# Kernel optimization log

Measured on AMD Instinct MI355X. Metric: run time of the kernel, lower is better.

## Reference

```python
import jax, jax.numpy as jnp
import numpy as np

B, T, D = 2, 1024, 2048
E, K, H = 64, 4, 512          # n_experts, top-k, expert_dim
S, HS = 2, H * K              # shared experts, shared hidden dim
CAP = 512


def setup_inputs() -> dict:
    key = jax.random.key(0)
    ks = jax.random.split(key, 9)
    scale = 0.02
    return {
        "x": jax.random.normal(ks[0], (B, T, D), jnp.float32),
        "Wr": jax.random.normal(ks[1], (D, E), jnp.float32) * scale,
        "router_bias": jnp.zeros((E,), jnp.float32),
        "Wg": jax.random.normal(ks[2], (E, D, H), jnp.float32) * scale,
        "Wu": jax.random.normal(ks[3], (E, D, H), jnp.float32) * scale,
        "Wd": jax.random.normal(ks[4], (E, H, D), jnp.float32) * scale,
        "Sg": jax.random.normal(ks[5], (S, D, HS), jnp.float32) * scale,
        "Su": jax.random.normal(ks[6], (S, D, HS), jnp.float32) * scale,
        "Sd": jax.random.normal(ks[7], (S, HS, D), jnp.float32) * scale,
    }


def reference(x, Wr, router_bias, Wg, Wu, Wd, Sg, Su, Sd):
    Bx, Tx, Dx = x.shape
    N = Bx * Tx
    flat = x.reshape(N, Dx)                              # [N, D]

    # ---- router ----
    logits = flat @ Wr + router_bias                     # [N, E]
    scores = jax.nn.softmax(logits, axis=-1)
    topk_scores, topk_idx = jax.lax.top_k(scores, K)     # [N, K]
    topk_scores = topk_scores / topk_scores.sum(-1, keepdims=True)

    eid = topk_idx.reshape(-1)                           # [N*K] expert per assignment
    w = topk_scores.reshape(-1)                          # [N*K] combine weight
    tok = jnp.repeat(jnp.arange(N), K)                   # [N*K] source token id

    # position of each assignment within its expert's buffer
    oh = jax.nn.one_hot(eid, E, dtype=jnp.int32)         # [N*K, E]
    pos = ((jnp.cumsum(oh, axis=0) * oh).sum(-1) - 1)    # [N*K]
    valid = pos < CAP

    # ---- dispatch: scatter tokens into per-expert buffers ----
    xb = jnp.zeros((E, CAP, Dx), x.dtype).at[eid, pos].set(flat[tok], mode="drop")

    # ---- grouped SwiGLU expert FFN ----
    h = jax.nn.silu(jnp.einsum("ecd,edh->ech", xb, Wg)) * jnp.einsum("ecd,edh->ech", xb, Wu)
    yb = jnp.einsum("ech,ehd->ecd", h, Wd)               # [E, CAP, D]

    # ---- combine: gather back and weighted scatter-add to tokens ----
    y = yb[eid, jnp.minimum(pos, CAP - 1)] * (w * valid)[:, None]
    out = jnp.zeros((N, Dx), x.dtype).at[tok].add(y)

    # ---- always-on shared experts ----
    hs = jax.nn.silu(jnp.einsum("nd,sdh->nsh", flat, Sg)) * jnp.einsum("nd,sdh->nsh", flat, Su)
    out = out + jnp.einsum("nsh,shd->nd", hs, Sd)

    return out.reshape(Bx, Tx, Dx)
```

## Files before the change

### kernel.cpp

```cpp
#include <hip/hip_runtime.h>
#include <hip/hip_bf16.h>
#include <stdint.h>

#define N_TOK 2048
#define DM    2048
#define NEXP  64
#define TOPK  4
#define HEXP  512
#define CAPC  512
#define NSH   2
#define HSH   2048
#define RTB   8

typedef __attribute__((ext_vector_type(8))) short short8;
typedef __attribute__((ext_vector_type(4))) float f32x4;
typedef __attribute__((ext_vector_type(4))) float f4;
typedef __attribute__((ext_vector_type(4))) unsigned uint4v;

#define GLDS16(g, l) __builtin_amdgcn_global_load_lds(                     \
    (const __attribute__((address_space(1))) void*)(g),                    \
    (__attribute__((address_space(3))) void*)(l), 16, 0, 0)

#define VMWAIT(N) asm volatile("s_waitcnt vmcnt(" #N ")" ::: "memory")
#define BARX() do { asm volatile("" ::: "memory");                          \
                    __builtin_amdgcn_s_barrier();                           \
                    asm volatile("" ::: "memory"); } while (0)

static __device__ __forceinline__ unsigned short f2bf(float f) {
  union { float f; unsigned u; } v; v.f = f;
  unsigned r = v.u + 0x7FFFu + ((v.u >> 16) & 1u);
  return (unsigned short)(r >> 16);
}

static __device__ __forceinline__ unsigned pk2(float lo, float hi) {
  unsigned u;
  asm("v_cvt_pk_bf16_f32 %0, %1, %2" : "=v"(u) : "v"(lo), "v"(hi));
  return u;
}

__global__ __launch_bounds__(256) void k_convert(const float* __restrict__ x,
                                                 unsigned short* __restrict__ xb) {
  int i = (blockIdx.x * 256 + threadIdx.x) * 8;
  f4 a = *(const f4*)(x + i);
  f4 b = *(const f4*)(x + i + 4);
  short8 o;
  o[0]=f2bf(a[0]); o[1]=f2bf(a[1]); o[2]=f2bf(a[2]); o[3]=f2bf(a[3]);
  o[4]=f2bf(b[0]); o[5]=f2bf(b[1]); o[6]=f2bf(b[2]); o[7]=f2bf(b[3]);
  *(short8*)(xb + i) = o;
}

#define ARGMAX_ROUND(S,I)                                            \
  { float bv = v; int bi = lane;                                     \
    _Pragma("unroll")                                                \
    for (int o = 32; o; o >>= 1) {                                   \
      float ov = __shfl_xor(bv, o); int oi = __shfl_xor(bi, o);      \
      if (ov > bv || (ov == bv && oi < bi)) { bv = ov; bi = oi; }    \
    }                                                                \
    S = bv; I = bi; if (lane == bi) v = -1.f; }

__global__ __launch_bounds__(256) void k_router(const float* __restrict__ x,
    const float* __restrict__ Wr, const float* __restrict__ bias,
    int* __restrict__ cnt, int* __restrict__ lists, float* __restrict__ wlist) {
  __shared__ float part[4][RTB][64];
  __shared__ float logits[RTB][64];
  int t = threadIdx.x;
  int e = t & 63, sl = t >> 6;
  int tok0 = blockIdx.x * RTB;
  const float* xp = x + (size_t)tok0 * DM;
  float acc[RTB];
#pragma unroll
  for (int i = 0; i < RTB; ++i) acc[i] = 0.f;
  for (int d = sl * 512; d < sl * 512 + 512; ++d) {
    float w = Wr[(size_t)d * NEXP + e];
#pragma unroll
    for (int i = 0; i < RTB; ++i) acc[i] += xp[(size_t)i * DM + d] * w;
  }
#pragma unroll
  for (int i = 0; i < RTB; ++i) part[sl][i][e] = acc[i];
  __syncthreads();
  for (int i = sl; i < RTB; i += 4)
    logits[i][e] = part[0][i][e] + part[1][i][e] + part[2][i][e] + part[3][i][e] + bias[e];
  __syncthreads();
  int lane = t & 63, wv = t >> 6;
  for (int i = wv * 2; i < wv * 2 + 2; ++i) {
    float lg = logits[i][lane];
    float m = lg;
#pragma unroll
    for (int o = 32; o; o >>= 1) m = fmaxf(m, __shfl_xor(m, o));
    float p = expf(lg - m);
    float sm = p;
#pragma unroll
    for (int o = 32; o; o >>= 1) sm += __shfl_xor(sm, o);
    float v = p / sm;
    float s0, s1, s2, s3; int i0, i1, i2, i3;
    ARGMAX_ROUND(s0, i0)
    ARGMAX_ROUND(s1, i1)
    ARGMAX_ROUND(s2, i2)
    ARGMAX_ROUND(s3, i3)
    float tot = s0 + s1 + s2 + s3;
    if (lane < TOPK) {
      float myw = (lane == 0 ? s0 : lane == 1 ? s1 : lane == 2 ? s2 : s3) / tot;
      int   mye = (lane == 0 ? i0 : lane == 1 ? i1 : lane == 2 ? i2 : i3);
      int pos = atomicAdd(&cnt[mye], 1);
      if (pos < CAPC) {
        lists[mye * CAPC + pos] = tok0 + i;
        wlist[mye * CAPC + pos] = myw;
      }
    }
  }
}

__global__ void k_offs(const int* __restrict__ cnt, int* __restrict__ offs) {
  int l = threadIdx.x;
  int c = min(cnt[l], CAPC);
  int sum = c;
#pragma unroll
  for (int o = 1; o < 64; o <<= 1) {
    int ov = __shfl_up(sum, o);
    if (l >= o) sum += ov;
  }
  offs[l + 1] = sum;
  if (l == 0) offs[0] = 0;
}

static __device__ __forceinline__ short8 frag_ldA(const unsigned short* lds, int row, int kElem) {
  int byte = row * 64 + kElem * 2;
  byte ^= ((row >> 1) & 3) << 4;
  return *(const short8*)((const char*)lds + byte);
}

static __device__ __forceinline__ short8 bfragB(const float* lB, int nl, int kb) {
  const float* p = lB + kb * 64 + (nl ^ (((kb >> 3) & 1) << 4));
  float f0 = p[0],   f1 = p[64],  f2 = p[128], f3 = p[192];
  float f4_ = p[256], f5 = p[320], f6 = p[384], f7 = p[448];
  uint4v uv = { pk2(f0, f1), pk2(f2, f3), pk2(f4_, f5), pk2(f6, f7) };
  return __builtin_bit_cast(short8, uv);
}

static __device__ __forceinline__ void mma1f(const unsigned short* lA, const float* lB,
    f32x4 (&acc)[4][2], int wm, int wn, int lane) {
  int r16 = lane & 15;
  int kb  = (lane >> 4) * 8;
  short8 a[4], b[2];
#pragma unroll
  for (int mf = 0; mf < 4; ++mf) a[mf] = frag_ldA(lA, wm + mf * 16 + r16, kb);
#pragma unroll
  for (int nf = 0; nf < 2; ++nf) b[nf] = bfragB(lB, wn + nf * 16 + r16, kb);
#pragma unroll
  for (int mf = 0; mf < 4; ++mf)
#pragma unroll
    for (int nf = 0; nf < 2; ++nf)
      acc[mf][nf] = __builtin_amdgcn_mfma_f32_16x16x32_bf16(a[mf], b[nf], acc[mf][nf], 0, 0, 0);
}

static __device__ __forceinline__ float silu_mul(float g, float u) {
  return g / (1.f + expf(-g)) * u;
}

#define A_SETUP(asrc, SROW_EXPR)                                            \
  const unsigned short* asrc[2];                                            \
  {                                                                         \
    _Pragma("unroll")                                                       \
    for (int p = 0; p < 2; ++p) {                                           \
      int row = p * 64 + wv * 16 + (lane >> 2);                             \
      int srow = (SROW_EXPR);                                               \
      asrc[p] = Abase + (size_t)srow * lda                                  \
              + (((lane & 3) ^ ((row >> 1) & 3)) << 3);                     \
    }                                                                       \
  }
#define A_STAGE(asrc, lAbuf, k0)                                            \
  { _Pragma("unroll")                                                       \
    for (int p = 0; p < 2; ++p)                                             \
      GLDS16(asrc[p] + (k0), (lAbuf) + p * 2048 + wv * 512); }

#define B_SETUP(bsrc, Bbase, ldb)                                           \
  const float* bsrc[2];                                                     \
  {                                                                         \
    _Pragma("unroll")                                                       \
    for (int p = 0; p < 2; ++p) {                                           \
      int k = p * 16 + wv * 4 + (lane >> 4);                                \
      int c = (lane & 15) ^ (((k >> 3) & 1) << 2);                          \
      bsrc[p] = (Bbase) + (size_t)k * (ldb) + n0 + c * 4;                   \
    }                                                                       \
  }
#define B_STAGE(bsrc, lBbuf, k0, ldb)                                       \
  { _Pragma("unroll")                                                       \
    for (int p = 0; p < 2; ++p)                                             \
      GLDS16(bsrc[p] + (size_t)(k0) * (ldb), (lBbuf) + p * 1024 + wv * 256); }

#define MM_STEP(q, tn, LDB)                                                 \
  VMWAIT(12); BARX();                                                       \
  mma1f(lA[q], lB[q], acc, wm, wn, lane);                                   \
  BARX();                                                                   \
  A_STAGE(asrc, lA[q], (tn) * 32)                                           \
  B_STAGE(bsrc, lB[q], (tn) * 32, LDB)

#define MM_PEEL(q, W)                                                       \
  VMWAIT(W); BARX();                                                        \
  mma1f(lA[q], lB[q], acc, wm, wn, lane);

__global__ __launch_bounds__(256, 2) void k_mmE(const unsigned short* __restrict__ xbf,
    const float* __restrict__ Wg, const float* __restrict__ Wu,
    const int* __restrict__ cnt, const int* __restrict__ offs,
    const int* __restrict__ lists, unsigned short* __restrict__ hg,
    unsigned short* __restrict__ hu) {
  int bid = blockIdx.x;
  int e   = ((bid & 7) << 3) | ((bid >> 3) & 7);
  int nb  = (bid >> 6) & 7;
  int mat = bid >> 9;
  int n0 = nb * 64;
  int ne = min(cnt[e], CAPC);
  if (ne == 0) return;
  const float* B = (mat ? Wu : Wg) + (size_t)e * DM * HEXP;
  unsigned short* hdst = mat ? hu : hg;
  const int* lst = lists + e * CAPC;
  int base = offs[e];
  __shared__ unsigned short lA[4][128 * 32];
  __shared__ float lB[4][32 * 64];
  int tid = threadIdx.x, lane = tid & 63, wv = tid >> 6;
  int wm = (wv >> 1) * 64, wn = (wv & 1) * 32;
  const unsigned short* Abase = xbf; const int lda = DM;
  B_SETUP(bsrc, B, HEXP)
  const int NT = DM / 32;
  for (int m0 = 0; m0 < ne; m0 += 128) {
    A_SETUP(asrc, lst[min(m0 + row, ne - 1)])
    f32x4 acc[4][2] = {};
#pragma unroll
    for (int q = 0; q < 4; ++q) {
      A_STAGE(asrc, lA[q], q * 32)
      B_STAGE(bsrc, lB[q], q * 32, HEXP)
    }
#pragma unroll 1
    for (int t = 0; t < NT - 4; t += 4) {
      MM_STEP(0, t + 4, HEXP)
      MM_STEP(1, t + 5, HEXP)
      MM_STEP(2, t + 6, HEXP)
      MM_STEP(3, t + 7, HEXP)
    }
    MM_PEEL(0, 12) MM_PEEL(1, 8) MM_PEEL(2, 4) MM_PEEL(3, 0)
    BARX();
#pragma unroll
    for (int mf = 0; mf < 4; ++mf)
#pragma unroll
      for (int r = 0; r < 4; ++r) {
        int rl = m0 + wm + mf * 16 + (lane >> 4) * 4 + r;
        if (rl < ne) {
#pragma unroll
          for (int nf = 0; nf < 2; ++nf) {
            int col = n0 + wn + nf * 16 + (lane & 15);
            hdst[(size_t)(base + rl) * HEXP + col] = f2bf(acc[mf][nf][r]);
          }
        }
      }
  }
}

__global__ __launch_bounds__(256) void k_swiglu_e(const unsigned short* __restrict__ hg,
    const unsigned short* __restrict__ hu, const int* __restrict__ offs,
    unsigned short* __restrict__ hws) {
  int total = offs[NEXP];
  int gid = blockIdx.x * 256 + threadIdx.x;
  int row = gid >> 6;
  if (row >= total) return;
  int c0 = (gid & 63) * 8;
  size_t o = (size_t)row * HEXP + c0;
  short8 g8 = *(const short8*)(hg + o);
  short8 u8 = *(const short8*)(hu + o);
  short8 r;
#pragma unroll
  for (int j = 0; j < 8; ++j) {
    union { unsigned u; float f; } gg, uu;
    gg.u = ((unsigned)(unsigned short)g8[j]) << 16;
    uu.u = ((unsigned)(unsigned short)u8[j]) << 16;
    r[j] = f2bf(silu_mul(gg.f, uu.f));
  }
  *(short8*)(hws + o) = r;
}

__global__ __launch_bounds__(256, 2) void k_mmS(const unsigned short* __restrict__ xbf,
    const float* __restrict__ Sg, const float* __restrict__ Su,
    unsigned short* __restrict__ hsg, unsigned short* __restrict__ hsu) {
  int bid = blockIdx.x;
  int nb = bid & 31, mb = (bid >> 5) & 15, s = (bid >> 9) & 1, mat = bid >> 10;
  int n0 = nb * 64, m0 = mb * 128;
  const float* B = (mat ? Su : Sg) + (size_t)s * DM * HSH;
  unsigned short* hdst = mat ? hsu : hsg;
  __shared__ unsigned short lA[4][128 * 32];
  __shared__ float lB[4][32 * 64];
  int tid = threadIdx.x, lane = tid & 63, wv = tid >> 6;
  int wm = (wv >> 1) * 64, wn = (wv & 1) * 32;
  const unsigned short* Abase = xbf; const int lda = DM;
  B_SETUP(bsrc, B, HSH)
  A_SETUP(asrc, m0 + row)
  f32x4 acc[4][2] = {};
  const int NT = DM / 32;
#pragma unroll
  for (int q = 0; q < 4; ++q) {
    A_STAGE(asrc, lA[q], q * 32)
    B_STAGE(bsrc, lB[q], q * 32, HSH)
  }
#pragma unroll 1
  for (int t = 0; t < NT - 4; t += 4) {
    MM_STEP(0, t + 4, HSH)
    MM_STEP(1, t + 5, HSH)
    MM_STEP(2, t + 6, HSH)
    MM_STEP(3, t + 7, HSH)
  }
  MM_PEEL(0, 12) MM_PEEL(1, 8) MM_PEEL(2, 4) MM_PEEL(3, 0)
#pragma unroll
  for (int mf = 0; mf < 4; ++mf)
#pragma unroll
    for (int nf = 0; nf < 2; ++nf)
#pragma unroll
      for (int r = 0; r < 4; ++r) {
        int row = m0 + wm + mf * 16 + (lane >> 4) * 4 + r;
        int col = n0 + wn + nf * 16 + (lane & 15);
        hdst[(size_t)row * (NSH * HSH) + s * HSH + col] = f2bf(acc[mf][nf][r]);
      }
}

__global__ __launch_bounds__(256) void k_swiglu_s(const unsigned short* __restrict__ hsg,
    const unsigned short* __restrict__ hsu, unsigned short* __restrict__ hs) {
  int gid = blockIdx.x * 256 + threadIdx.x;
  size_t o = (size_t)gid * 8;
  short8 g8 = *(const short8*)(hsg + o);
  short8 u8 = *(const short8*)(hsu + o);
  short8 r;
#pragma unroll
  for (int j = 0; j < 8; ++j) {
    union { unsigned u; float f; } gg, uu;
    gg.u = ((unsigned)(unsigned short)g8[j]) << 16;
    uu.u = ((unsigned)(unsigned short)u8[j]) << 16;
    r[j] = f2bf(silu_mul(gg.f, uu.f));
  }
  *(short8*)(hs + o) = r;
}

__global__ __launch_bounds__(256, 2) void k_sd4(const unsigned short* __restrict__ hs,
    const float* __restrict__ Sd, float* __restrict__ out) {
  int bid = blockIdx.x;
  int nb = bid & 31, mb = bid >> 5;
  int n0 = nb * 64, m0 = mb * 128;
  __shared__ unsigned short lA[4][128 * 32];
  __shared__ float lB[4][32 * 64];
  int tid = threadIdx.x, lane = tid & 63, wv = tid >> 6;
  int wm = (wv >> 1) * 64, wn = (wv & 1) * 32;
  const unsigned short* Abase = hs; const int lda = NSH * HSH;
  B_SETUP(bsrc, Sd, DM)
  A_SETUP(asrc, m0 + row)
  f32x4 acc[4][2] = {};
  const int NT = (NSH * HSH) / 32;
#pragma unroll
  for (int q = 0; q < 4; ++q) {
    A_STAGE(asrc, lA[q], q * 32)
    B_STAGE(bsrc, lB[q], q * 32, DM)
  }
#pragma unroll 1
  for (int t = 0; t < NT - 4; t += 4) {
    MM_STEP(0, t + 4, DM)
    MM_STEP(1, t + 5, DM)
    MM_STEP(2, t + 6, DM)
    MM_STEP(3, t + 7, DM)
  }
  MM_PEEL(0, 12) MM_PEEL(1, 8) MM_PEEL(2, 4) MM_PEEL(3, 0)
#pragma unroll
  for (int mf = 0; mf < 4; ++mf)
#pragma unroll
    for (int nf = 0; nf < 2; ++nf)
#pragma unroll
      for (int r = 0; r < 4; ++r) {
        int row = m0 + wm + mf * 16 + (lane >> 4) * 4 + r;
        int col = n0 + wn + nf * 16 + (lane & 15);
        out[(size_t)row * DM + col] = acc[mf][nf][r];
      }
}

__global__ __launch_bounds__(256, 2) void k_downE(const unsigned short* __restrict__ hws,
    const float* __restrict__ Wd, const int* __restrict__ cnt, const int* __restrict__ offs,
    const int* __restrict__ lists, const float* __restrict__ wlist,
    float* __restrict__ out) {
  int bid = blockIdx.x;
  int e  = ((bid & 7) << 3) | ((bid >> 3) & 7);
  int nb = bid >> 6;
  int n0 = nb * 64;
  int ne = min(cnt[e], CAPC);
  if (ne == 0) return;
  const float* B = Wd + (size_t)e * HEXP * DM;
  __shared__ unsigned short lA[4][128 * 32];
  __shared__ float lB[4][32 * 64];
  int tid = threadIdx.x, lane = tid & 63, wv = tid >> 6;
  int wm = (wv >> 1) * 64, wn = (wv & 1) * 32;
  const unsigned short* Abase = hws + (size_t)offs[e] * HEXP; const int lda = HEXP;
  B_SETUP(bsrc, B, DM)
  const int NT = HEXP / 32;
  for (int m0 = 0; m0 < ne; m0 += 128) {
    A_SETUP(asrc, min(m0 + row, ne - 1))
    f32x4 acc[4][2] = {};
#pragma unroll
    for (int q = 0; q < 4; ++q) {
      A_STAGE(asrc, lA[q], q * 32)
      B_STAGE(bsrc, lB[q], q * 32, DM)
    }
#pragma unroll 1
    for (int t = 0; t < NT - 4; t += 4) {
      MM_STEP(0, t + 4, DM)
      MM_STEP(1, t + 5, DM)
      MM_STEP(2, t + 6, DM)
      MM_STEP(3, t + 7, DM)
    }
    MM_PEEL(0, 12) MM_PEEL(1, 8) MM_PEEL(2, 4) MM_PEEL(3, 0)
    BARX();
#pragma unroll
    for (int mf = 0; mf < 4; ++mf)
#pragma unroll
      for (int r = 0; r < 4; ++r) {
        int rl = m0 + wm + mf * 16 + (lane >> 4) * 4 + r;
        if (rl < ne) {
          int tok  = lists[e * CAPC + rl];
          float w  = wlist[e * CAPC + rl];
#pragma unroll
          for (int nf = 0; nf < 2; ++nf) {
            int col = n0 + wn + nf * 16 + (lane & 15);
            atomicAdd(out + (size_t)tok * DM + col, acc[mf][nf][r] * w);
          }
        }
      }
  }
}

extern "C" void kernel_launch(void* const* d_in, const int* in_sizes, int n_in,
                              void* d_out, int out_size, void* d_ws, size_t ws_size,
                              hipStream_t stream) {
  const float* x    = (const float*)d_in[0];
  const float* Wr   = (const float*)d_in[1];
  const float* bias = (const float*)d_in[2];
  const float* Wg   = (const float*)d_in[3];
  const float* Wu   = (const float*)d_in[4];
  const float* Wd   = (const float*)d_in[5];
  const float* Sg   = (const float*)d_in[6];
  const float* Su   = (const float*)d_in[7];
  const float* Sd   = (const float*)d_in[8];
  float* out = (float*)d_out;
  char* ws = (char*)d_ws;

  const size_t off_cnt   = 0;
  const size_t off_offs  = 256;
  const size_t off_lists = 1024;
  const size_t off_wlist = off_lists + (size_t)NEXP * CAPC * 4;
  const size_t off_xbf   = off_wlist + (size_t)NEXP * CAPC * 4;
  const size_t off_hs    = off_xbf + (size_t)N_TOK * DM * 2;
  const size_t off_hws   = off_hs + (size_t)N_TOK * NSH * HSH * 2;
  const size_t off_hg    = off_hws + (size_t)N_TOK * TOPK * HEXP * 2;
  const size_t off_hu    = off_hg + (size_t)N_TOK * TOPK * HEXP * 2;
  const size_t off_hsg   = off_hu + (size_t)N_TOK * TOPK * HEXP * 2;
  const size_t off_hsu   = off_hsg + (size_t)N_TOK * NSH * HSH * 2;
  const size_t req       = off_hsu + (size_t)N_TOK * NSH * HSH * 2;
  if (ws_size < req) return;

  int* cnt            = (int*)(ws + off_cnt);
  int* offs           = (int*)(ws + off_offs);
  int* lists          = (int*)(ws + off_lists);
  float* wlist        = (float*)(ws + off_wlist);
  unsigned short* xbf = (unsigned short*)(ws + off_xbf);
  unsigned short* hs  = (unsigned short*)(ws + off_hs);
  unsigned short* hws = (unsigned short*)(ws + off_hws);
  unsigned short* hg  = (unsigned short*)(ws + off_hg);
  unsigned short* hu  = (unsigned short*)(ws + off_hu);
  unsigned short* hsg = (unsigned short*)(ws + off_hsg);
  unsigned short* hsu = (unsigned short*)(ws + off_hsu);

  hipMemsetAsync(cnt, 0, NEXP * sizeof(int), stream);
  k_convert<<<(N_TOK * DM) / (256 * 8), 256, 0, stream>>>(x, xbf);
  k_router<<<N_TOK / RTB, 256, 0, stream>>>(x, Wr, bias, cnt, lists, wlist);
  k_offs<<<1, 64, 0, stream>>>(cnt, offs);

  k_mmE<<<1024, 256, 0, stream>>>(xbf, Wg, Wu, cnt, offs, lists, hg, hu);
  k_swiglu_e<<<(N_TOK * TOPK * HEXP / 8) / 256, 256, 0, stream>>>(hg, hu, offs, hws);

  k_mmS<<<2048, 256, 0, stream>>>(xbf, Sg, Su, hsg, hsu);
  k_swiglu_s<<<(N_TOK * NSH * HSH / 8) / 256, 256, 0, stream>>>(hsg, hsu, hs);

  k_sd4<<<512, 256, 0, stream>>>(hs, Sd, out);
  k_downE<<<2048, 256, 0, stream>>>(hws, Wd, cnt, offs, lists, wlist, out);
}
```

Baseline: 712.2 us.

## Replace direct global-to-LDS staging with register-prefetched double-buffered LDS pipeline

All four GEMM kernels drop the global_load_lds path with four LDS stages. Each thread now prefetches four k-tiles into registers and writes them into two LDS buffers before each MFMA step. LDS use is halved, and launch bounds move from 2 to 3 blocks per CU to raise occupancy. The cost is extra VGPRs for the prefetch registers, explicit ds_write plus lgkmcnt waits, and a single barrier per step. With only two LDS buffers, that single barrier may leave a write-after-read hazard between steps.

```diff
diff --git a/kernel.cpp b/kernel.cpp
--- a/kernel.cpp
+++ b/kernel.cpp
@@ -17,11 +17,8 @@
 typedef __attribute__((ext_vector_type(4))) float f4;
 typedef __attribute__((ext_vector_type(4))) unsigned uint4v;
 
-#define GLDS16(g, l) __builtin_amdgcn_global_load_lds(                     \
-    (const __attribute__((address_space(1))) void*)(g),                    \
-    (__attribute__((address_space(3))) void*)(l), 16, 0, 0)
-
 #define VMWAIT(N) asm volatile("s_waitcnt vmcnt(" #N ")" ::: "memory")
+#define LGKM0()   asm volatile("s_waitcnt lgkmcnt(0)" ::: "memory")
 #define BARX() do { asm volatile("" ::: "memory");                          \
                     __builtin_amdgcn_s_barrier();                           \
                     asm volatile("" ::: "memory"); } while (0)
@@ -157,49 +154,55 @@
   return g / (1.f + expf(-g)) * u;
 }
 
-#define A_SETUP(asrc, SROW_EXPR)                                            \
-  const unsigned short* asrc[2];                                            \
-  {                                                                         \
-    _Pragma("unroll")                                                       \
-    for (int p = 0; p < 2; ++p) {                                           \
-      int row = p * 64 + wv * 16 + (lane >> 2);                             \
-      int srow = (SROW_EXPR);                                               \
-      asrc[p] = Abase + (size_t)srow * lda                                  \
-              + (((lane & 3) ^ ((row >> 1) & 3)) << 3);                     \
-    }                                                                       \
-  }
-#define A_STAGE(asrc, lAbuf, k0)                                            \
-  { _Pragma("unroll")                                                       \
-    for (int p = 0; p < 2; ++p)                                             \
-      GLDS16(asrc[p] + (k0), (lAbuf) + p * 2048 + wv * 512); }
-
-#define B_SETUP(bsrc, Bbase, ldb)                                           \
-  const float* bsrc[2];                                                     \
-  {                                                                         \
-    _Pragma("unroll")                                                       \
-    for (int p = 0; p < 2; ++p) {                                           \
-      int k = p * 16 + wv * 4 + (lane >> 4);                                \
-      int c = (lane & 15) ^ (((k >> 3) & 1) << 2);                          \
-      bsrc[p] = (Bbase) + (size_t)k * (ldb) + n0 + c * 4;                   \
-    }                                                                       \
-  }
-#define B_STAGE(bsrc, lBbuf, k0, ldb)                                       \
-  { _Pragma("unroll")                                                       \
-    for (int p = 0; p < 2; ++p)                                             \
-      GLDS16(bsrc[p] + (size_t)(k0) * (ldb), (lBbuf) + p * 1024 + wv * 256); }
-
-#define MM_STEP(q, tn, LDB)                                                 \
-  VMWAIT(12); BARX();                                                       \
-  mma1f(lA[q], lB[q], acc, wm, wn, lane);                                   \
-  BARX();                                                                   \
-  A_STAGE(asrc, lA[q], (tn) * 32)                                           \
-  B_STAGE(bsrc, lB[q], (tn) * 32, LDB)
-
-#define MM_PEEL(q, W)                                                       \
-  VMWAIT(W); BARX();                                                        \
-  mma1f(lA[q], lB[q], acc, wm, wn, lane);
-
-__global__ __launch_bounds__(256, 2) void k_mmE(const unsigned short* __restrict__ xbf,
+
+#define ENG_SETUP()                                                         \
+  int tid = threadIdx.x, lane = tid & 63, wv = tid >> 6;                    \
+  int wm = (wv >> 1) * 64, wn = (wv & 1) * 32;                              \
+  int arow = tid >> 1;                                                      \
+  int ac   = (tid & 1) * 2;                                                 \
+  int aswz = ((arow >> 1) & 3) << 4;                                        \
+  int awb0 = arow * 64 + ((ac * 16) ^ aswz);                                \
+  int awb1 = arow * 64 + (((ac + 1) * 16) ^ aswz);                          \
+  int bk   = tid >> 3;                                                      \
+  int bc   = (tid & 7) * 2;                                                 \
+  int bswz = ((bk >> 3) & 1) << 2;                                          \
+  int bwb0 = bk * 64 + ((bc ^ bswz) << 2);                                  \
+  int bwb1 = bk * 64 + (((bc + 1) ^ bswz) << 2);
+
+#define LOADT(q, t, LDB)                                                    \
+  ar0[q] = *(const short8*)(aptr + (size_t)(t) * 32);                       \
+  ar1[q] = *(const short8*)(aptr + (size_t)(t) * 32 + 8);                   \
+  br0[q] = *(const f4*)(bptr + (size_t)(t) * 32 * (LDB));                   \
+  br1[q] = *(const f4*)(bptr + (size_t)(t) * 32 * (LDB) + 4);
+
+#define WRT(q)                                                              \
+  *(short8*)((char*)(lA[(q) & 1]) + awb0) = ar0[q];                         \
+  *(short8*)((char*)(lA[(q) & 1]) + awb1) = ar1[q];                         \
+  *(f4*)(lB[(q) & 1] + bwb0) = br0[q];                                      \
+  *(f4*)(lB[(q) & 1] + bwb1) = br1[q];
+
+#define PHS(q, t, LDB)                                                      \
+  VMWAIT(12);                                                               \
+  WRT(q)                                                                    \
+  LGKM0(); BARX();                                                          \
+  mma1f(lA[(q) & 1], lB[(q) & 1], acc, wm, wn, lane);                       \
+  LOADT(q, (t) + 4, LDB)
+
+#define PHE(q, WN)                                                          \
+  VMWAIT(WN);                                                               \
+  WRT(q)                                                                    \
+  LGKM0(); BARX();                                                          \
+  mma1f(lA[(q) & 1], lB[(q) & 1], acc, wm, wn, lane);
+
+#define KLOOP(NT, LDB)                                                      \
+  LOADT(0, 0, LDB) LOADT(1, 1, LDB) LOADT(2, 2, LDB) LOADT(3, 3, LDB)       \
+  _Pragma("unroll 1")                                                       \
+  for (int t = 0; t < (NT) - 4; t += 4) {                                   \
+    PHS(0, t, LDB) PHS(1, t + 1, LDB) PHS(2, t + 2, LDB) PHS(3, t + 3, LDB) \
+  }                                                                         \
+  PHE(0, 12) PHE(1, 8) PHE(2, 4) PHE(3, 0)
+
+__global__ __launch_bounds__(256, 3) void k_mmE(const unsigned short* __restrict__ xbf,
     const float* __restrict__ Wg, const float* __restrict__ Wu,
     const int* __restrict__ cnt, const int* __restrict__ offs,
     const int* __restrict__ lists, unsigned short* __restrict__ hg,
@@ -215,30 +218,16 @@
   unsigned short* hdst = mat ? hu : hg;
   const int* lst = lists + e * CAPC;
   int base = offs[e];
-  __shared__ unsigned short lA[4][128 * 32];
-  __shared__ float lB[4][32 * 64];
-  int tid = threadIdx.x, lane = tid & 63, wv = tid >> 6;
-  int wm = (wv >> 1) * 64, wn = (wv & 1) * 32;
-  const unsigned short* Abase = xbf; const int lda = DM;
-  B_SETUP(bsrc, B, HEXP)
-  const int NT = DM / 32;
+  __shared__ unsigned short lA[2][128 * 32];
+  __shared__ float lB[2][32 * 64];
+  ENG_SETUP()
+  const float* bptr = B + (size_t)bk * HEXP + n0 + bc * 4;
+  short8 ar0[4], ar1[4]; f4 br0[4], br1[4];
   for (int m0 = 0; m0 < ne; m0 += 128) {
-    A_SETUP(asrc, lst[min(m0 + row, ne - 1)])
+    int srow = lst[min(m0 + arow, ne - 1)];
+    const unsigned short* aptr = xbf + (size_t)srow * DM + ac * 8;
     f32x4 acc[4][2] = {};
-#pragma unroll
-    for (int q = 0; q < 4; ++q) {
-      A_STAGE(asrc, lA[q], q * 32)
-      B_STAGE(bsrc, lB[q], q * 32, HEXP)
-    }
-#pragma unroll 1
-    for (int t = 0; t < NT - 4; t += 4) {
-      MM_STEP(0, t + 4, HEXP)
-      MM_STEP(1, t + 5, HEXP)
-      MM_STEP(2, t + 6, HEXP)
-      MM_STEP(3, t + 7, HEXP)
-    }
-    MM_PEEL(0, 12) MM_PEEL(1, 8) MM_PEEL(2, 4) MM_PEEL(3, 0)
-    BARX();
+    KLOOP(64, HEXP)
 #pragma unroll
     for (int mf = 0; mf < 4; ++mf)
 #pragma unroll
@@ -277,7 +266,7 @@
   *(short8*)(hws + o) = r;
 }
 
-__global__ __launch_bounds__(256, 2) void k_mmS(const unsigned short* __restrict__ xbf,
+__global__ __launch_bounds__(256, 3) void k_mmS(const unsigned short* __restrict__ xbf,
     const float* __restrict__ Sg, const float* __restrict__ Su,
     unsigned short* __restrict__ hsg, unsigned short* __restrict__ hsu) {
   int bid = blockIdx.x;
@@ -285,28 +274,14 @@
   int n0 = nb * 64, m0 = mb * 128;
   const float* B = (mat ? Su : Sg) + (size_t)s * DM * HSH;
   unsigned short* hdst = mat ? hsu : hsg;
-  __shared__ unsigned short lA[4][128 * 32];
-  __shared__ float lB[4][32 * 64];
-  int tid = threadIdx.x, lane = tid & 63, wv = tid >> 6;
-  int wm = (wv >> 1) * 64, wn = (wv & 1) * 32;
-  const unsigned short* Abase = xbf; const int lda = DM;
-  B_SETUP(bsrc, B, HSH)
-  A_SETUP(asrc, m0 + row)
+  __shared__ unsigned short lA[2][128 * 32];
+  __shared__ float lB[2][32 * 64];
+  ENG_SETUP()
+  const float* bptr = B + (size_t)bk * HSH + n0 + bc * 4;
+  const unsigned short* aptr = xbf + (size_t)(m0 + arow) * DM + ac * 8;
+  short8 ar0[4], ar1[4]; f4 br0[4], br1[4];
   f32x4 acc[4][2] = {};
-  const int NT = DM / 32;
-#pragma unroll
-  for (int q = 0; q < 4; ++q) {
-    A_STAGE(asrc, lA[q], q * 32)
-    B_STAGE(bsrc, lB[q], q * 32, HSH)
-  }
-#pragma unroll 1
-  for (int t = 0; t < NT - 4; t += 4) {
-    MM_STEP(0, t + 4, HSH)
-    MM_STEP(1, t + 5, HSH)
-    MM_STEP(2, t + 6, HSH)
-    MM_STEP(3, t + 7, HSH)
-  }
-  MM_PEEL(0, 12) MM_PEEL(1, 8) MM_PEEL(2, 4) MM_PEEL(3, 0)
+  KLOOP(64, HSH)
 #pragma unroll
   for (int mf = 0; mf < 4; ++mf)
 #pragma unroll
@@ -336,33 +311,19 @@
   *(short8*)(hs + o) = r;
 }
 
-__global__ __launch_bounds__(256, 2) void k_sd4(const unsigned short* __restrict__ hs,
+__global__ __launch_bounds__(256, 3) void k_sd4(const unsigned short* __restrict__ hs,
     const float* __restrict__ Sd, float* __restrict__ out) {
   int bid = blockIdx.x;
   int nb = bid & 31, mb = bid >> 5;
   int n0 = nb * 64, m0 = mb * 128;
-  __shared__ unsigned short lA[4][128 * 32];
-  __shared__ float lB[4][32 * 64];
-  int tid = threadIdx.x, lane = tid & 63, wv = tid >> 6;
-  int wm = (wv >> 1) * 64, wn = (wv & 1) * 32;
-  const unsigned short* Abase = hs; const int lda = NSH * HSH;
-  B_SETUP(bsrc, Sd, DM)
-  A_SETUP(asrc, m0 + row)
+  __shared__ unsigned short lA[2][128 * 32];
+  __shared__ float lB[2][32 * 64];
+  ENG_SETUP()
+  const float* bptr = Sd + (size_t)bk * DM + n0 + bc * 4;
+  const unsigned short* aptr = hs + (size_t)(m0 + arow) * (NSH * HSH) + ac * 8;
+  short8 ar0[4], ar1[4]; f4 br0[4], br1[4];
   f32x4 acc[4][2] = {};
-  const int NT = (NSH * HSH) / 32;
-#pragma unroll
-  for (int q = 0; q < 4; ++q) {
-    A_STAGE(asrc, lA[q], q * 32)
-    B_STAGE(bsrc, lB[q], q * 32, DM)
-  }
-#pragma unroll 1
-  for (int t = 0; t < NT - 4; t += 4) {
-    MM_STEP(0, t + 4, DM)
-    MM_STEP(1, t + 5, DM)
-    MM_STEP(2, t + 6, DM)
-    MM_STEP(3, t + 7, DM)
-  }
-  MM_PEEL(0, 12) MM_PEEL(1, 8) MM_PEEL(2, 4) MM_PEEL(3, 0)
+  KLOOP(128, DM)
 #pragma unroll
   for (int mf = 0; mf < 4; ++mf)
 #pragma unroll
@@ -375,7 +336,7 @@
       }
 }
 
-__global__ __launch_bounds__(256, 2) void k_downE(const unsigned short* __restrict__ hws,
+__global__ __launch_bounds__(256, 3) void k_downE(const unsigned short* __restrict__ hws,
     const float* __restrict__ Wd, const int* __restrict__ cnt, const int* __restrict__ offs,
     const int* __restrict__ lists, const float* __restrict__ wlist,
     float* __restrict__ out) {
@@ -386,30 +347,16 @@
   int ne = min(cnt[e], CAPC);
   if (ne == 0) return;
   const float* B = Wd + (size_t)e * HEXP * DM;
-  __shared__ unsigned short lA[4][128 * 32];
-  __shared__ float lB[4][32 * 64];
-  int tid = threadIdx.x, lane = tid & 63, wv = tid >> 6;
-  int wm = (wv >> 1) * 64, wn = (wv & 1) * 32;
-  const unsigned short* Abase = hws + (size_t)offs[e] * HEXP; const int lda = HEXP;
-  B_SETUP(bsrc, B, DM)
-  const int NT = HEXP / 32;
+  const unsigned short* Abase = hws + (size_t)offs[e] * HEXP;
+  __shared__ unsigned short lA[2][128 * 32];
+  __shared__ float lB[2][32 * 64];
+  ENG_SETUP()
+  const float* bptr = B + (size_t)bk * DM + n0 + bc * 4;
+  short8 ar0[4], ar1[4]; f4 br0[4], br1[4];
   for (int m0 = 0; m0 < ne; m0 += 128) {
-    A_SETUP(asrc, min(m0 + row, ne - 1))
+    const unsigned short* aptr = Abase + (size_t)min(m0 + arow, ne - 1) * HEXP + ac * 8;
     f32x4 acc[4][2] = {};
-#pragma unroll
-    for (int q = 0; q < 4; ++q) {
-      A_STAGE(asrc, lA[q], q * 32)
-      B_STAGE(bsrc, lB[q], q * 32, DM)
-    }
-#pragma unroll 1
-    for (int t = 0; t < NT - 4; t += 4) {
-      MM_STEP(0, t + 4, DM)
-      MM_STEP(1, t + 5, DM)
-      MM_STEP(2, t + 6, DM)
-      MM_STEP(3, t + 7, DM)
-    }
-    MM_PEEL(0, 12) MM_PEEL(1, 8) MM_PEEL(2, 4) MM_PEEL(3, 0)
-    BARX();
+    KLOOP(16, DM)
 #pragma unroll
     for (int mf = 0; mf < 4; ++mf)
 #pragma unroll
```

Measured after the change: 759.9 us. 6.7% more time.
